# Kernel optimization log

Measured on AMD Instinct MI355X. Metric: run time of the kernel, lower is better.

## Reference

```python
import jax, jax.numpy as jnp
import numpy as np

B, S, V, H = 1, 2048, 1024, 16
D = V // H  # head_size = 64


def setup_inputs() -> dict:
    key = jax.random.key(0)
    ks = jax.random.split(key, 7)
    s = 1.0 / np.sqrt(V)  # keep logits in a sane range
    return {
        "x": jax.random.normal(ks[0], (B, S, V), jnp.float32),
        "W_qkv": (jax.random.normal(ks[1], (3 * V, V), jnp.float32) * s),
        "W_out": (jax.random.normal(ks[2], (V, V), jnp.float32) * s),
        "W_pos": (jax.random.normal(ks[3], (V, V), jnp.float32) * s),
        "u_vec": (jax.random.normal(ks[4], (1, H, 1, D), jnp.float32) * 0.02),
        "v_vec": (jax.random.normal(ks[5], (1, H, 1, D), jnp.float32) * 0.02),
        "rel_embed": jax.random.normal(ks[6], (S, V), jnp.float32),
    }


def reference(x, W_qkv, W_out, W_pos, u_vec, v_vec, rel_embed):
    b, s, _ = x.shape
    # qkv projection (nn.Linear, no bias): x @ W.T, then split into q,k,v
    qkv = x @ W_qkv.T
    q, k, v = jnp.split(qkv, 3, axis=-1)
    to_heads = lambda t: t.reshape(b, s, H, D).transpose(0, 2, 1, 3)  # [B,H,S,D]
    q, k, v = to_heads(q), to_heads(k), to_heads(v)

    # content term: (q + u) @ k^T  -> [B,H,S,S]
    attn_dots = jnp.einsum('bhid,bhjd->bhij', q + u_vec, k)

    # relative-position term: Linear(rel_embed).T viewed as [H, D, S]
    rel = (rel_embed @ W_pos.T).T.reshape(H, D, s)
    query_posn = jnp.einsum('bhid,hdj->bhij', q + v_vec, rel)  # [B,H,S,S]

    # Transformer-XL style shift-gather: out[i, j] = in[i, (j - i - 1) mod S]
    col_idx = ((-jnp.arange(s))[:, None] + jnp.arange(s)[None, :] - 1) % s
    shifted = jnp.take_along_axis(query_posn, col_idx[None, None, :, :], axis=-1)

    causal_mask = jnp.triu(jnp.ones((s, s), dtype=bool), k=1)  # True above diagonal
    dots = jnp.where(causal_mask, -jnp.inf, attn_dots + shifted) / np.sqrt(D)
    scores = jax.nn.softmax(dots, axis=-1)

    attn = jnp.einsum('bhij,bhjd->bhid', scores, v)
    out = attn.transpose(0, 2, 1, 3).reshape(b, s, V) @ W_out.T
    return out
```

## Files before the change

### kernel.cpp

```cpp
#include <hip/hip_runtime.h>
#include <math.h>

#define S 2048
#define H 16
#define D 64
#define V 1024

typedef float f32x4 __attribute__((ext_vector_type(4)));
typedef __bf16 bf16x8 __attribute__((ext_vector_type(8)));
typedef unsigned short u16;

#define GLOBAL_AS __attribute__((address_space(1)))
#define LDS_AS __attribute__((address_space(3)))

__device__ __forceinline__ u16 f2bf(float x) {
    unsigned u = __float_as_uint(x);
    u = u + 0x7FFFu + ((u >> 16) & 1u);
    return (u16)(u >> 16);
}
__device__ __forceinline__ float bf2f(u16 b) {
    return __uint_as_float(((unsigned)b) << 16);
}

#if __has_builtin(__builtin_amdgcn_global_load_lds)
#define HAS_ASYNC 1
#endif

__device__ __forceinline__ void async_ld16(const u16* g, u16* ldsu, int lane) {
#ifdef HAS_ASYNC
    auto gp = reinterpret_cast<GLOBAL_AS void*>(reinterpret_cast<uintptr_t>(g));
    auto lp = reinterpret_cast<LDS_AS void*>(reinterpret_cast<uintptr_t>(ldsu));
    __builtin_amdgcn_global_load_lds(gp, lp, 16, 0, 0);
#else
    *(uint4*)((char*)ldsu + lane * 16) = *(const uint4*)g;
#endif
}

__global__ __launch_bounds__(256) void prep5(
    const float* __restrict__ a0, u16* __restrict__ b0, int n0,
    const float* __restrict__ a1, u16* __restrict__ b1, int n1,
    const float* __restrict__ a2, u16* __restrict__ b2, int n2,
    const float* __restrict__ a3, u16* __restrict__ b3, int n3,
    const float* __restrict__ a4, u16* __restrict__ b4, int n4)
{
    const int tot = n0 + n1 + n2 + n3 + n4;
    for (int i = blockIdx.x * 256 + threadIdx.x; i < tot; i += gridDim.x * 256) {
        const float* s; u16* d; int j = i;
        if (j < n0) { s = a0; d = b0; }
        else if ((j -= n0) < n1) { s = a1; d = b1; }
        else if ((j -= n1) < n2) { s = a2; d = b2; }
        else if ((j -= n2) < n3) { s = a3; d = b3; }
        else { j -= n3; s = a4; d = b4; }
        float4 f = ((const float4*)s)[j];
        ((ushort4*)d)[j] = make_ushort4(f2bf(f.x), f2bf(f.y), f2bf(f.z), f2bf(f.w));
    }
}

__global__ __launch_bounds__(256) void gemm_proj(
    const u16* __restrict__ x_h, const u16* __restrict__ rel_h,
    const u16* __restrict__ Wq_h, const u16* __restrict__ Wpos_h,
    u16* __restrict__ qk_h, u16* __restrict__ Vt_g, u16* __restrict__ P_h)
{
    __shared__ u16 A_s[128 * 32];
    __shared__ u16 B_s[128 * 32];

    const int bid = blockIdx.x;
    const bool g1 = bid < 384;
    const int m0 = (g1 ? (bid / 24) : ((bid - 384) / 8)) * 128;
    const int n0 = (g1 ? (bid % 24) : ((bid - 384) % 8)) * 128;
    const u16* Ag = g1 ? x_h : rel_h;
    const u16* Bg = g1 ? Wq_h : Wpos_h;

    const int tid = threadIdx.x;
    const int lane = tid & 63;
    const int w = tid >> 6;
    const int wm = (w & 1) * 64, wn = (w >> 1) * 64;
    const int fr = lane & 15;
    const int fq = lane >> 4;
    const int lr = lane >> 2, lc = (lane & 3) * 8;

    f32x4 acc[4][4] = {};

    for (int k0 = 0; k0 < 1024; k0 += 32) {
        __syncthreads();
#pragma unroll
        for (int i = 0; i < 2; ++i) {
            const int r0 = w * 32 + i * 16;
            async_ld16(Ag + (size_t)(m0 + r0 + lr) * 1024 + k0 + lc, A_s + r0 * 32, lane);
            async_ld16(Bg + (size_t)(n0 + r0 + lr) * 1024 + k0 + lc, B_s + r0 * 32, lane);
        }
        __syncthreads();

        bf16x8 a[4], b[4];
#pragma unroll
        for (int t = 0; t < 4; ++t) {
            a[t] = *(const bf16x8*)&A_s[(wm + t * 16 + fr) * 32 + fq * 8];
            b[t] = *(const bf16x8*)&B_s[(wn + t * 16 + fr) * 32 + fq * 8];
        }
#pragma unroll
        for (int mi = 0; mi < 4; ++mi)
#pragma unroll
            for (int ni = 0; ni < 4; ++ni)
                acc[mi][ni] = __builtin_amdgcn_mfma_f32_16x16x32_bf16(
                    a[mi], b[ni], acc[mi][ni], 0, 0, 0);
    }

    const int er = fq * 4;
    if (g1 && n0 >= 2048) {
#pragma unroll
        for (int mi = 0; mi < 4; ++mi)
#pragma unroll
            for (int ni = 0; ni < 4; ++ni) {
                const int col = n0 - 2048 + wn + ni * 16 + fr;
                const int mrow = m0 + wm + mi * 16 + er;
                *(ushort4*)&Vt_g[(size_t)col * 2048 + mrow] = make_ushort4(
                    f2bf(acc[mi][ni][0]), f2bf(acc[mi][ni][1]),
                    f2bf(acc[mi][ni][2]), f2bf(acc[mi][ni][3]));
            }
    } else {
        u16* Cb = g1 ? qk_h : P_h;
        const int ldc = g1 ? 2048 : 1024;
#pragma unroll
        for (int mi = 0; mi < 4; ++mi)
#pragma unroll
            for (int ni = 0; ni < 4; ++ni)
#pragma unroll
                for (int g = 0; g < 4; ++g)
                    Cb[(size_t)(m0 + wm + mi * 16 + er + g) * ldc + n0 + wn + ni * 16 + fr] =
                        f2bf(acc[mi][ni][g]);
    }
}

__global__ __launch_bounds__(256, 3) void attn_mfma(
    const u16* __restrict__ qk_h, const u16* __restrict__ Vt_g,
    const u16* __restrict__ P_h,
    const float* __restrict__ u_vec, const float* __restrict__ v_vec,
    u16* __restrict__ O_h)
{
    const int h = blockIdx.y;
    const int tile = ((blockIdx.y >> 3) & 1) ? blockIdx.x : (gridDim.x - 1 - blockIdx.x);
    const int i0 = tile * 64;
    const int tid = threadIdx.x;
    const int lane = tid & 63;
    const int w = tid >> 6;
    const int fr = lane & 15;
    const int fq = lane >> 4;

    __shared__ u16 K_s[64 * 72];
    __shared__ u16 Vt_s[64 * 72];
    __shared__ u16 P_s[128 * 72];
    __shared__ u16 p_s[64 * 72];

    bf16x8 qu[2], qv[2];
    {
        const int row = i0 + w * 16 + fr;
        const int base = h * 64 + fq * 8;
#pragma unroll
        for (int c = 0; c < 2; ++c) {
            bf16x8 q8 = *(const bf16x8*)(qk_h + (size_t)row * 2048 + base + c * 32);
            float4 u0 = *(const float4*)(u_vec + base + c * 32);
            float4 u1 = *(const float4*)(u_vec + base + c * 32 + 4);
            float4 v0 = *(const float4*)(v_vec + base + c * 32);
            float4 v1 = *(const float4*)(v_vec + base + c * 32 + 4);
            const float uf[8] = {u0.x, u0.y, u0.z, u0.w, u1.x, u1.y, u1.z, u1.w};
            const float vf[8] = {v0.x, v0.y, v0.z, v0.w, v1.x, v1.y, v1.z, v1.w};
#pragma unroll
            for (int j = 0; j < 8; ++j) {
                const float qf = (float)q8[j];
                qu[c][j] = (__bf16)(qf + uf[j]);
                qv[c][j] = (__bf16)(qf + vf[j]);
            }
        }
    }

    const int rKV = tid >> 2;
    const int cKV = (tid & 3) * 16;
    const int rP = tid >> 1;
    const int cP = (tid & 1) * 32;

    uint4 pfK0, pfK1, pfV0, pfV1, pfP0, pfP1, pfP2, pfP3;
    auto load_pf = [&](int j0) {
        const u16* kg = qk_h + (size_t)(j0 + rKV) * 2048 + 1024 + h * 64 + cKV;
        pfK0 = *(const uint4*)kg;
        pfK1 = *(const uint4*)(kg + 8);
        const u16* vg = Vt_g + (size_t)(h * 64 + rKV) * 2048 + j0 + cKV;
        pfV0 = *(const uint4*)vg;
        pfV1 = *(const uint4*)(vg + 8);
        int prow = S + j0 - i0 - 64 + rP;
        if (prow > S - 1) prow = S - 1;
        const u16* pg = P_h + (size_t)prow * 1024 + h * 64 + cP;
        pfP0 = *(const uint4*)pg;
        pfP1 = *(const uint4*)(pg + 8);
        pfP2 = *(const uint4*)(pg + 16);
        pfP3 = *(const uint4*)(pg + 24);
    };

    f32x4 O[4] = {};
    float l[4] = {};

    const int tbase = 3 - w;
    const int bsh = 15 - fq * 4;

    load_pf(0);

    for (int j0 = 0; j0 <= i0; j0 += 64) {
        __syncthreads();
        *(uint4*)&K_s[rKV * 72 + cKV] = pfK0;
        *(uint4*)&K_s[rKV * 72 + cKV + 8] = pfK1;
        *(uint4*)&Vt_s[rKV * 72 + cKV] = pfV0;
        *(uint4*)&Vt_s[rKV * 72 + cKV + 8] = pfV1;
        *(uint4*)&P_s[rP * 72 + cP] = pfP0;
        *(uint4*)&P_s[rP * 72 + cP + 8] = pfP1;
        *(uint4*)&P_s[rP * 72 + cP + 16] = pfP2;
        *(uint4*)&P_s[rP * 72 + cP + 24] = pfP3;
        if (j0 + 64 <= i0) load_pf(j0 + 64);
        __syncthreads();

        f32x4 accQK[4] = {};
        f32x4 accQP[5] = {};
#pragma unroll
        for (int c = 0; c < 2; ++c) {
            const int kk = c * 32 + fq * 8;
#pragma unroll
            for (int nt = 0; nt < 4; ++nt) {
                bf16x8 b = *(const bf16x8*)&K_s[(nt * 16 + fr) * 72 + kk];
                accQK[nt] = __builtin_amdgcn_mfma_f32_16x16x32_bf16(qu[c], b, accQK[nt], 0, 0, 0);
            }
#pragma unroll
            for (int t = 0; t < 5; ++t) {
                bf16x8 b = *(const bf16x8*)&P_s[((tbase + t) * 16 + fr) * 72 + kk];
                accQP[t] = __builtin_amdgcn_mfma_f32_16x16x32_bf16(qv[c], b, accQP[t], 0, 0, 0);
            }
        }

        float p[4][4];
#pragma unroll
        for (int nt = 0; nt < 4; ++nt)
#pragma unroll
            for (int g = 0; g < 4; ++g) {
                const int b = bsh - g;
                const int srcfr = fr + b;
                const int srcLane = (fq << 4) | (srcfr & 15);
                const float lo = __shfl(accQP[nt][g], srcLane, 64);
                const float hi = __shfl(accQP[nt + 1][g], srcLane, 64);
                const float qp = (srcfr < 16) ? lo : hi;
                const int rr = w * 16 + fq * 4 + g;
                const int j = nt * 16 + fr;
                const float s = (accQK[nt][g] + qp) * 0.125f;
                const float e = ((j0 + j) <= (i0 + rr)) ? __expf(s) : 0.f;
                p[nt][g] = e;
                l[g] += e;
            }
#pragma unroll
        for (int nt = 0; nt < 4; ++nt)
#pragma unroll
            for (int g = 0; g < 4; ++g)
                p_s[(w * 16 + fq * 4 + g) * 72 + nt * 16 + fr] = f2bf(p[nt][g]);

#pragma unroll
        for (int c = 0; c < 2; ++c) {
            const int kk = c * 32 + fq * 8;
            bf16x8 a = *(const bf16x8*)&p_s[(w * 16 + fr) * 72 + kk];
#pragma unroll
            for (int nt = 0; nt < 4; ++nt) {
                bf16x8 b = *(const bf16x8*)&Vt_s[(nt * 16 + fr) * 72 + kk];
                O[nt] = __builtin_amdgcn_mfma_f32_16x16x32_bf16(a, b, O[nt], 0, 0, 0);
            }
        }
    }

#pragma unroll
    for (int g = 0; g < 4; ++g)
#pragma unroll
        for (int off = 1; off < 16; off <<= 1)
            l[g] += __shfl_xor(l[g], off, 64);

#pragma unroll
    for (int nt = 0; nt < 4; ++nt)
#pragma unroll
        for (int g = 0; g < 4; ++g) {
            const int rr = w * 16 + fq * 4 + g;
            O_h[(size_t)(i0 + rr) * 1024 + h * 64 + nt * 16 + fr] = f2bf(O[nt][g] / l[g]);
        }
}

__global__ __launch_bounds__(256) void gemm_out(
    const u16* __restrict__ O_g, const u16* __restrict__ Wout_h,
    float* __restrict__ C)
{
    __shared__ u16 A_s[128 * 32];
    __shared__ u16 B_s[64 * 32];

    const int tid = threadIdx.x;
    const int lane = tid & 63;
    const int w = tid >> 6;
    const int m0 = blockIdx.y * 128, n0 = blockIdx.x * 64;
    const int wm = (w & 1) * 64, wn = (w >> 1) * 32;
    const int fr = lane & 15;
    const int fq = lane >> 4;
    const int lr = lane >> 2, lc = (lane & 3) * 8;

    f32x4 acc[4][2] = {};

    for (int k0 = 0; k0 < 1024; k0 += 32) {
        __syncthreads();
#pragma unroll
        for (int i = 0; i < 2; ++i) {
            const int r0 = w * 32 + i * 16;
            async_ld16(O_g + (size_t)(m0 + r0 + lr) * 1024 + k0 + lc, A_s + r0 * 32, lane);
        }
        async_ld16(Wout_h + (size_t)(n0 + w * 16 + lr) * 1024 + k0 + lc,
                   B_s + w * 16 * 32, lane);
        __syncthreads();

        bf16x8 a[4], b[2];
#pragma unroll
        for (int t = 0; t < 4; ++t)
            a[t] = *(const bf16x8*)&A_s[(wm + t * 16 + fr) * 32 + fq * 8];
#pragma unroll
        for (int t = 0; t < 2; ++t)
            b[t] = *(const bf16x8*)&B_s[(wn + t * 16 + fr) * 32 + fq * 8];
#pragma unroll
        for (int mi = 0; mi < 4; ++mi)
#pragma unroll
            for (int ni = 0; ni < 2; ++ni)
                acc[mi][ni] = __builtin_amdgcn_mfma_f32_16x16x32_bf16(
                    a[mi], b[ni], acc[mi][ni], 0, 0, 0);
    }

    const int er = fq * 4;
#pragma unroll
    for (int mi = 0; mi < 4; ++mi)
#pragma unroll
        for (int ni = 0; ni < 2; ++ni)
#pragma unroll
            for (int g = 0; g < 4; ++g)
                C[(size_t)(m0 + wm + mi * 16 + er + g) * 1024 + n0 + wn + ni * 16 + fr] =
                    acc[mi][ni][g];
}

extern "C" void kernel_launch(void* const* d_in, const int* in_sizes, int n_in,
                              void* d_out, int out_size, void* d_ws, size_t ws_size,
                              hipStream_t stream) {
    const float* x     = (const float*)d_in[0];
    const float* W_qkv = (const float*)d_in[1];
    const float* W_out = (const float*)d_in[2];
    const float* W_pos = (const float*)d_in[3];
    const float* u_vec = (const float*)d_in[4];
    const float* v_vec = (const float*)d_in[5];
    const float* rel   = (const float*)d_in[6];
    float* out = (float*)d_out;

    char* ws = (char*)d_ws;
    u16* x_h    = (u16*)(ws);
    u16* rel_h  = (u16*)(ws + 4194304);
    u16* Wq_h   = (u16*)(ws + 8388608);
    u16* Wpos_h = (u16*)(ws + 14680064);
    u16* Wout_h = (u16*)(ws + 16777216);
    u16* qk_h   = (u16*)(ws + 18874368);
    u16* Vt_g   = (u16*)(ws + 27262976);
    u16* P_h    = (u16*)(ws + 31457280);
    u16* O_h    = (u16*)(ws + 35651584);

    prep5<<<dim3(2048), dim3(256), 0, stream>>>(
        x, x_h, 2048 * 1024 / 4,
        rel, rel_h, 2048 * 1024 / 4,
        W_qkv, Wq_h, 3072 * 1024 / 4,
        W_pos, Wpos_h, 1024 * 1024 / 4,
        W_out, Wout_h, 1024 * 1024 / 4);

    gemm_proj<<<dim3(512), dim3(256), 0, stream>>>(
        x_h, rel_h, Wq_h, Wpos_h, qk_h, Vt_g, P_h);

    attn_mfma<<<dim3(32, 16), dim3(256), 0, stream>>>(
        qk_h, Vt_g, P_h, u_vec, v_vec, O_h);

    gemm_out<<<dim3(16, 16), dim3(256), 0, stream>>>(O_h, Wout_h, out);
}
```

Before: 194.8 us.

## Split causal attention over key chunks with atomic accumulation and separate normalization

Each query tile's key range is split into chunks of up to 512 keys, so the attention grid grows from 32 to 80 blocks per head and the long causal rows no longer dominate the tail. Partial unnormalized outputs and row sums are combined with float atomicAdd into zeroed scratch buffers, and a new attn_norm kernel divides by the sums and converts to bf16. The split is only correct because the softmax here has no per-chunk running max to reconcile. The cost is an extra memset, an extra kernel, and fp32 atomic traffic over the whole output. The next tile's prefetch is also moved to after the second barrier.

```diff
diff --git a/kernel.cpp b/kernel.cpp
--- a/kernel.cpp
+++ b/kernel.cpp
@@ -135,11 +135,20 @@
     const u16* __restrict__ qk_h, const u16* __restrict__ Vt_g,
     const u16* __restrict__ P_h,
     const float* __restrict__ u_vec, const float* __restrict__ v_vec,
-    u16* __restrict__ O_h)
+    float* __restrict__ O_acc, float* __restrict__ l_acc)
 {
     const int h = blockIdx.y;
-    const int tile = ((blockIdx.y >> 3) & 1) ? blockIdx.x : (gridDim.x - 1 - blockIdx.x);
-    const int i0 = tile * 64;
+    const int bx = blockIdx.x;
+    int ti, ck;
+    if (bx < 8)       { ti = bx;                                ck = 0; }
+    else if (bx < 24) { const int t = bx - 8;  ti = 8 + (t >> 1);  ck = t & 1; }
+    else if (bx < 48) { const int t = bx - 24; const int q = t / 3;
+                        ti = 16 + q;                            ck = t - 3 * q; }
+    else              { const int t = bx - 48; ti = 24 + (t >> 2); ck = t & 3; }
+    const int i0 = ti * 64;
+    const int j0s = ck * 512;
+    const int j0e = min(i0, j0s + 448);
+
     const int tid = threadIdx.x;
     const int lane = tid & 63;
     const int w = tid >> 6;
@@ -201,9 +210,9 @@
     const int tbase = 3 - w;
     const int bsh = 15 - fq * 4;
 
-    load_pf(0);
-
-    for (int j0 = 0; j0 <= i0; j0 += 64) {
+    load_pf(j0s);
+
+    for (int j0 = j0s; j0 <= j0e; j0 += 64) {
         __syncthreads();
         *(uint4*)&K_s[rKV * 72 + cKV] = pfK0;
         *(uint4*)&K_s[rKV * 72 + cKV + 8] = pfK1;
@@ -213,8 +222,8 @@
         *(uint4*)&P_s[rP * 72 + cP + 8] = pfP1;
         *(uint4*)&P_s[rP * 72 + cP + 16] = pfP2;
         *(uint4*)&P_s[rP * 72 + cP + 24] = pfP3;
-        if (j0 + 64 <= i0) load_pf(j0 + 64);
-        __syncthreads();
+        __syncthreads();
+        if (j0 + 64 <= j0e) load_pf(j0 + 64);
 
         f32x4 accQK[4] = {};
         f32x4 accQP[5] = {};
@@ -280,8 +289,25 @@
 #pragma unroll
         for (int g = 0; g < 4; ++g) {
             const int rr = w * 16 + fq * 4 + g;
-            O_h[(size_t)(i0 + rr) * 1024 + h * 64 + nt * 16 + fr] = f2bf(O[nt][g] / l[g]);
-        }
+            atomicAdd(&O_acc[(size_t)(i0 + rr) * 1024 + h * 64 + nt * 16 + fr], O[nt][g]);
+        }
+    if (fr == 0)
+#pragma unroll
+        for (int g = 0; g < 4; ++g)
+            atomicAdd(&l_acc[h * 2048 + i0 + w * 16 + fq * 4 + g], l[g]);
+}
+
+__global__ __launch_bounds__(256) void attn_norm(
+    const float* __restrict__ O_acc, const float* __restrict__ l_acc,
+    u16* __restrict__ O_h)
+{
+    const int idx = blockIdx.x * 256 + threadIdx.x;
+    const int row = idx >> 8;
+    const int hh = (idx & 255) >> 4;
+    const float inv = 1.0f / l_acc[hh * 2048 + row];
+    float4 o = ((const float4*)O_acc)[idx];
+    ((ushort4*)O_h)[idx] = make_ushort4(
+        f2bf(o.x * inv), f2bf(o.y * inv), f2bf(o.z * inv), f2bf(o.w * inv));
 }
 
 __global__ __launch_bounds__(256) void gemm_out(
@@ -361,6 +387,8 @@
     u16* Vt_g   = (u16*)(ws + 27262976);
     u16* P_h    = (u16*)(ws + 31457280);
     u16* O_h    = (u16*)(ws + 35651584);
+    float* O_acc = (float*)(ws);
+    float* l_acc = (float*)(ws + 8388608);
 
     prep5<<<dim3(2048), dim3(256), 0, stream>>>(
         x, x_h, 2048 * 1024 / 4,
@@ -372,8 +400,12 @@
     gemm_proj<<<dim3(512), dim3(256), 0, stream>>>(
         x_h, rel_h, Wq_h, Wpos_h, qk_h, Vt_g, P_h);
 
-    attn_mfma<<<dim3(32, 16), dim3(256), 0, stream>>>(
-        qk_h, Vt_g, P_h, u_vec, v_vec, O_h);
+    hipMemsetAsync(ws, 0, 8388608 + 131072, stream);
+
+    attn_mfma<<<dim3(80, 16), dim3(256), 0, stream>>>(
+        qk_h, Vt_g, P_h, u_vec, v_vec, O_acc, l_acc);
+
+    attn_norm<<<dim3(2048), dim3(256), 0, stream>>>(O_acc, l_acc, O_h);
 
     gemm_out<<<dim3(16, 16), dim3(256), 0, stream>>>(O_h, Wout_h, out);
 }
```

Measured after the change: 198.0 us. About the same (+1.6%).
